# Optimization experiments

Measured on AMD Instinct MI355X. Metric: run time of the kernel, lower is better.

The kernel has to match this reference:

```python
import jax, jax.numpy as jnp
import numpy as np

N_ROIS = 1024
C, H, W = 512, 38, 50           # VGG16 conv5 feature map for a 608x800 image (stride 16)
IMG_H, IMG_W = 608.0, 800.0
POOLING_SIZE = 7                 # cfg.POOLING_SIZE


def setup_inputs() -> dict:
    key = jax.random.key(0)
    k1, k2 = jax.random.split(key, 2)
    bottom = jax.random.normal(k1, (1, C, H, W), dtype=jnp.float32)
    # Build valid ROI boxes (batch_idx, x1, y1, x2, y2) in image coordinates.
    u = jax.random.uniform(k2, (N_ROIS, 4), dtype=jnp.float32)
    x1 = u[:, 0] * (IMG_W - 32.0)
    y1 = u[:, 1] * (IMG_H - 32.0)
    x2 = x1 + 16.0 + u[:, 2] * (IMG_W - 16.0 - x1)
    y2 = y1 + 16.0 + u[:, 3] * (IMG_H - 16.0 - y1)
    rois = jnp.stack([jnp.zeros(N_ROIS, jnp.float32), x1, y1, x2, y2], axis=1)
    return {"bottom": bottom, "rois": rois, "pooling_size": POOLING_SIZE}


def _crop_pool(bottom, rois, pooling_size):
    """Faithful jax version of Network._crop_pool_layer (max_pool=True).
    affine_grid + grid_sample use align_corners=True semantics (old PyTorch
    default, which this theta parameterization assumes) with zeros padding.
    """
    Cc, Hh, Ww = bottom.shape[1], bottom.shape[2], bottom.shape[3]
    pre = pooling_size * 2
    x1 = rois[:, 1] / 16.0
    y1 = rois[:, 2] / 16.0
    x2 = rois[:, 3] / 16.0
    y2 = rois[:, 4] / 16.0
    # theta (separable: grid-x depends only on output col, grid-y only on row)
    t00 = (x2 - x1) / (Ww - 1)
    t02 = (x1 + x2 - Ww + 1) / (Ww - 1)
    t11 = (y2 - y1) / (Hh - 1)
    t12 = (y1 + y2 - Hh + 1) / (Hh - 1)
    base = jnp.linspace(-1.0, 1.0, pre)                 # align_corners=True base grid
    gx = t00[:, None] * base[None, :] + t02[:, None]     # [N, pre] normalized x
    gy = t11[:, None] * base[None, :] + t12[:, None]     # [N, pre] normalized y
    ix = (gx + 1.0) * 0.5 * (Ww - 1)                     # input pixel coords
    iy = (gy + 1.0) * 0.5 * (Hh - 1)
    x0 = jnp.floor(ix)
    y0 = jnp.floor(iy)
    ax = ix - x0
    ay = iy - y0
    x0i = x0.astype(jnp.int32); x1i = x0i + 1
    y0i = y0.astype(jnp.int32); y1i = y0i + 1

    def clip_w(idx, w, size):  # zeros-padding: out-of-bounds corners contribute 0
        valid = (idx >= 0) & (idx <= size - 1)
        return jnp.clip(idx, 0, size - 1), jnp.where(valid, w, 0.0)

    x0c, wx0 = clip_w(x0i, 1.0 - ax, Ww)
    x1c, wx1 = clip_w(x1i, ax, Ww)
    y0c, wy0 = clip_w(y0i, 1.0 - ay, Hh)
    y1c, wy1 = clip_w(y1i, ay, Hh)

    imgf = bottom[0].reshape(Cc, Hh * Ww)               # single image, expanded in torch

    def corner(yc, xc, wy, wx):
        idx = yc[:, :, None] * Ww + xc[:, None, :]      # [N, pre, pre]
        v = jnp.take(imgf, idx, axis=1)                 # [C, N, pre, pre]
        return v * (wy[:, :, None] * wx[:, None, :])[None]

    crops = (corner(y0c, x0c, wy0, wx0) + corner(y0c, x1c, wy0, wx1)
             + corner(y1c, x0c, wy1, wx0) + corner(y1c, x1c, wy1, wx1))
    crops = jnp.transpose(crops, (1, 0, 2, 3))          # [N, C, pre, pre]
    n = rois.shape[0]
    # F.max_pool2d(crops, 2, 2)
    pooled = crops.reshape(n, Cc, pooling_size, 2, pooling_size, 2).max(axis=(3, 5))
    return pooled


def reference(bottom, rois, pooling_size):
    return _crop_pool(bottom, rois, pooling_size)
```

## Files before the change

### kernel.cpp

```cpp
#include <hip/hip_runtime.h>
#include <hip/hip_fp16.h>
#include <float.h>

#define C_    512
#define H_    38
#define W_    50
#define HW_   (H_ * W_)
#define NROIS 1024
#define PS    7
#define PRE   14
#define NCELL 49
#define CQ    128
#define NGP   (PRE * PRE)

typedef float vfloat4 __attribute__((ext_vector_type(4)));
typedef _Float16 h2 __attribute__((ext_vector_type(2)));

__device__ inline h2 bch2(int v)   { return __builtin_bit_cast(h2, v); }
__device__ inline h2 bch2u(unsigned v) { return __builtin_bit_cast(h2, v); }
__device__ inline int bcint(h2 v)  { return __builtin_bit_cast(int, v); }

__global__ __launch_bounds__(256) void transpose_kernel(
    const float* __restrict__ in, _Float16* __restrict__ out) {
    __shared__ float tile[32][33];
    const int pix0 = blockIdx.x * 32;
    const int c0   = blockIdx.y * 32;
    const int tx = threadIdx.x & 31;
    const int ty = threadIdx.x >> 5;

    for (int i = ty; i < 32; i += 8) {
        int c = c0 + i, pix = pix0 + tx;
        tile[i][tx] = (pix < HW_) ? in[c * HW_ + pix] : 0.0f;
    }
    __syncthreads();
    for (int i = ty; i < 32; i += 8) {
        int pix = pix0 + i, c = c0 + tx;
        if (pix < HW_) out[pix * C_ + c] = (_Float16)tile[tx][i];
    }
}

__global__ __launch_bounds__(256, 8) void croppool_kernel(
    const _Float16* __restrict__ src, const float* __restrict__ rois,
    float* __restrict__ out) {

    const int n  = blockIdx.x >> 2;
    const int cq = blockIdx.x & 3;
    const int cbase = cq * CQ;
    const int tid = threadIdx.x;

    __shared__ _Float16 outtile[CQ * NCELL];
    __shared__ int4  offt[NGP];
    __shared__ uint4 wgtt[NGP];

    if (tid < NGP) {
        const int gy = tid / PRE, gx = tid - PRE * gy;
        const float rx1 = rois[n * 5 + 1] * 0.0625f;
        const float ry1 = rois[n * 5 + 2] * 0.0625f;
        const float rx2 = rois[n * 5 + 3] * 0.0625f;
        const float ry2 = rois[n * 5 + 4] * 0.0625f;

        int xi0, xi1, yi0, yi1;
        float wx0, wx1, wy0, wy1;
        {
            const float sz = (float)(W_ - 1);
            const float t0 = (rx2 - rx1) / sz, tc = (rx1 + rx2 - sz) / sz;
            const float base = -1.0f + (float)gx * (2.0f / 13.0f);
            const float coord = (t0 * base + tc + 1.0f) * 0.5f * sz;
            const float f = floorf(coord), a = coord - f;
            const int i0 = (int)f, i1 = i0 + 1;
            wx0 = (i0 >= 0 && i0 <= W_ - 1) ? (1.0f - a) : 0.0f;
            wx1 = (i1 >= 0 && i1 <= W_ - 1) ? a : 0.0f;
            xi0 = min(max(i0, 0), W_ - 1);
            xi1 = min(max(i1, 0), W_ - 1);
        }
        {
            const float sz = (float)(H_ - 1);
            const float t0 = (ry2 - ry1) / sz, tc = (ry1 + ry2 - sz) / sz;
            const float base = -1.0f + (float)gy * (2.0f / 13.0f);
            const float coord = (t0 * base + tc + 1.0f) * 0.5f * sz;
            const float f = floorf(coord), a = coord - f;
            const int i0 = (int)f, i1 = i0 + 1;
            wy0 = (i0 >= 0 && i0 <= H_ - 1) ? (1.0f - a) : 0.0f;
            wy1 = (i1 >= 0 && i1 <= H_ - 1) ? a : 0.0f;
            yi0 = min(max(i0, 0), H_ - 1);
            yi1 = min(max(i1, 0), H_ - 1);
        }
        offt[tid] = make_int4((yi0 * W_ + xi0) * C_, (yi0 * W_ + xi1) * C_,
                              (yi1 * W_ + xi0) * C_, (yi1 * W_ + xi1) * C_);
        const _Float16 w0 = (_Float16)(wy0 * wx0);
        const _Float16 w1 = (_Float16)(wy0 * wx1);
        const _Float16 w2 = (_Float16)(wy1 * wx0);
        const _Float16 w3 = (_Float16)(wy1 * wx1);
        uint4 wv;
        wv.x = __builtin_bit_cast(unsigned, (h2){w0, w0});
        wv.y = __builtin_bit_cast(unsigned, (h2){w1, w1});
        wv.z = __builtin_bit_cast(unsigned, (h2){w2, w2});
        wv.w = __builtin_bit_cast(unsigned, (h2){w3, w3});
        wgtt[tid] = wv;
    }
    __syncthreads();

    const int m    = tid & 15;
    const int q    = (tid >> 4) & 3;
    const int wave = tid >> 6;
    const _Float16* srcc = src + cbase + 8 * m;

    for (int cell = wave; cell < NCELL; cell += 4) {
        const int py = cell / PS, px = cell - PS * py;
        const int gp = (2 * py + (q >> 1)) * PRE + 2 * px + (q & 1);

        const int4  o  = offt[gp];
        const uint4 wv = wgtt[gp];
        const h2 w0 = bch2u(wv.x), w1 = bch2u(wv.y);
        const h2 w2 = bch2u(wv.z), w3 = bch2u(wv.w);

        const uint4 v0 = *(const uint4*)(srcc + o.x);
        const uint4 v1 = *(const uint4*)(srcc + o.y);
        const uint4 v2 = *(const uint4*)(srcc + o.z);
        const uint4 v3 = *(const uint4*)(srcc + o.w);

        h2 a0 = w0 * bch2u(v0.x) + w1 * bch2u(v1.x) + w2 * bch2u(v2.x) + w3 * bch2u(v3.x);
        h2 a1 = w0 * bch2u(v0.y) + w1 * bch2u(v1.y) + w2 * bch2u(v2.y) + w3 * bch2u(v3.y);
        h2 a2 = w0 * bch2u(v0.z) + w1 * bch2u(v1.z) + w2 * bch2u(v2.z) + w3 * bch2u(v3.z);
        h2 a3 = w0 * bch2u(v0.w) + w1 * bch2u(v1.w) + w2 * bch2u(v2.w) + w3 * bch2u(v3.w);

        #pragma unroll
        for (int s = 16; s <= 32; s <<= 1) {
            a0 = __builtin_elementwise_max(a0, bch2(__shfl_xor(bcint(a0), s, 64)));
            a1 = __builtin_elementwise_max(a1, bch2(__shfl_xor(bcint(a1), s, 64)));
            a2 = __builtin_elementwise_max(a2, bch2(__shfl_xor(bcint(a2), s, 64)));
            a3 = __builtin_elementwise_max(a3, bch2(__shfl_xor(bcint(a3), s, 64)));
        }

        const h2 sel = (q == 0) ? a0 : (q == 1) ? a1 : (q == 2) ? a2 : a3;
        const int c0 = 8 * m + 2 * q;
        outtile[c0 * NCELL + cell]       = sel.x;
        outtile[(c0 + 1) * NCELL + cell] = sel.y;
    }
    __syncthreads();

    float* dstb = out + (size_t)n * (C_ * NCELL) + cbase * NCELL;
    const uint4* lsrc = (const uint4*)outtile;
    for (int g = tid; g < CQ * NCELL / 8; g += 256) {
        const uint4 p = lsrc[g];
        vfloat4 lo, hi;
        h2 h;
        h = bch2u(p.x); lo[0] = (float)h.x; lo[1] = (float)h.y;
        h = bch2u(p.y); lo[2] = (float)h.x; lo[3] = (float)h.y;
        h = bch2u(p.z); hi[0] = (float)h.x; hi[1] = (float)h.y;
        h = bch2u(p.w); hi[2] = (float)h.x; hi[3] = (float)h.y;
        __builtin_nontemporal_store(lo, (vfloat4*)(dstb + 8 * g));
        __builtin_nontemporal_store(hi, (vfloat4*)(dstb + 8 * g + 4));
    }
}

__global__ __launch_bounds__(256) void croppool_fallback(
    const float* __restrict__ src, const float* __restrict__ rois,
    float* __restrict__ out) {

    const int n  = blockIdx.x >> 2;
    const int cq = blockIdx.x & 3;
    const int cbase = cq * CQ;
    const int tid = threadIdx.x;

    __shared__ float outtile[CQ * NCELL];
    __shared__ int   xi0[PRE], xi1[PRE], yi0[PRE], yi1[PRE];
    __shared__ float xw0[PRE], xw1[PRE], yw0[PRE], yw1[PRE];

    if (tid < 2 * PRE) {
        const int  j   = tid % PRE;
        const bool isy = tid >= PRE;
        const float r1 = rois[n * 5 + (isy ? 2 : 1)] * 0.0625f;
        const float r2 = rois[n * 5 + (isy ? 4 : 3)] * 0.0625f;
        const float sz = isy ? (float)(H_ - 1) : (float)(W_ - 1);
        const int  szi = isy ? (H_ - 1) : (W_ - 1);
        const float t0 = (r2 - r1) / sz;
        const float tc = (r1 + r2 - sz) / sz;
        const float base = -1.0f + (float)j * (2.0f / 13.0f);
        const float coord = (t0 * base + tc + 1.0f) * 0.5f * sz;
        const float f = floorf(coord);
        const float a = coord - f;
        const int i0 = (int)f;
        const int i1 = i0 + 1;
        const float w0 = (i0 >= 0 && i0 <= szi) ? (1.0f - a) : 0.0f;
        const float w1 = (i1 >= 0 && i1 <= szi) ? a : 0.0f;
        const int i0c = min(max(i0, 0), szi);
        const int i1c = min(max(i1, 0), szi);
        if (isy) { yi0[j] = i0c; yi1[j] = i1c; yw0[j] = w0; yw1[j] = w1; }
        else     { xi0[j] = i0c; xi1[j] = i1c; xw0[j] = w0; xw1[j] = w1; }
    }
    __syncthreads();

    const int wave = tid >> 6;
    const int lane = tid & 63;
    const float* srcc = src + (size_t)(cbase + lane) * HW_;

    for (int cell = wave; cell < NCELL; cell += 4) {
        const int py = cell / PS, px = cell % PS;
        float m0 = -FLT_MAX, m1 = -FLT_MAX;
        for (int ry = 0; ry < 2; ++ry) {
            const int gy = 2 * py + ry;
            for (int rx = 0; rx < 2; ++rx) {
                const int gx = 2 * px + rx;
                const int i00 = yi0[gy] * W_ + xi0[gx], i01 = yi0[gy] * W_ + xi1[gx];
                const int i10 = yi1[gy] * W_ + xi0[gx], i11 = yi1[gy] * W_ + xi1[gx];
                const float v0 = yw0[gy] * (xw0[gx] * srcc[i00] + xw1[gx] * srcc[i01])
                               + yw1[gy] * (xw0[gx] * srcc[i10] + xw1[gx] * srcc[i11]);
                const float v1 = yw0[gy] * (xw0[gx] * srcc[64 * HW_ + i00] + xw1[gx] * srcc[64 * HW_ + i01])
                               + yw1[gy] * (xw0[gx] * srcc[64 * HW_ + i10] + xw1[gx] * srcc[64 * HW_ + i11]);
                m0 = fmaxf(m0, v0);
                m1 = fmaxf(m1, v1);
            }
        }
        outtile[lane * NCELL + cell]        = m0;
        outtile[(lane + 64) * NCELL + cell] = m1;
    }
    __syncthreads();

    const vfloat4* lsrc = (const vfloat4*)outtile;
    vfloat4* dst = (vfloat4*)out + (size_t)n * (C_ * NCELL / 4) + cq * (CQ * NCELL / 4);
    for (int i = tid; i < CQ * NCELL / 4; i += 256) {
        __builtin_nontemporal_store(lsrc[i], &dst[i]);
    }
}

extern "C" void kernel_launch(void* const* d_in, const int* in_sizes, int n_in,
                              void* d_out, int out_size, void* d_ws, size_t ws_size,
                              hipStream_t stream) {
    const float* bottom = (const float*)d_in[0];
    const float* rois   = (const float*)d_in[1];
    float* out = (float*)d_out;

    const size_t trans_bytes = (size_t)HW_ * C_ * sizeof(_Float16);
    if (ws_size >= trans_bytes) {
        _Float16* trans = (_Float16*)d_ws;
        dim3 tgrid((HW_ + 31) / 32, C_ / 32);
        transpose_kernel<<<tgrid, 256, 0, stream>>>(bottom, trans);
        croppool_kernel<<<NROIS * 4, 256, 0, stream>>>(trans, rois, out);
    } else {
        croppool_fallback<<<NROIS * 4, 256, 0, stream>>>(bottom, rois, out);
    }
}
```

Baseline: 46.56 us.

## Process one ROI per 512-thread block with in-thread 2x2 max pooling

The crop-pool kernel now gives each block a whole ROI across all 512 channels with 512 threads, where each lane owns 8 channels and computes all four bilinear samples of a pooling cell itself. This replaces the cross-lane shuffle max reduction and removes the 4x redundant per-block grid/weight setup across channel quarters. The output tile is stored cell-major in a padded LDS buffer and transposed on write-out with scalar fp32 nontemporal stores. The trade-offs are higher register pressure from 16 outstanding 16-byte loads per iteration, scalar rather than vector global stores, and fewer, larger blocks.

```diff
diff --git a/kernel.cpp b/kernel.cpp
--- a/kernel.cpp
+++ b/kernel.cpp
@@ -10,15 +10,14 @@
 #define PS    7
 #define PRE   14
 #define NCELL 49
-#define CQ    128
 #define NGP   (PRE * PRE)
+#define OTP   516
 
 typedef float vfloat4 __attribute__((ext_vector_type(4)));
 typedef _Float16 h2 __attribute__((ext_vector_type(2)));
 
-__device__ inline h2 bch2(int v)   { return __builtin_bit_cast(h2, v); }
-__device__ inline h2 bch2u(unsigned v) { return __builtin_bit_cast(h2, v); }
-__device__ inline int bcint(h2 v)  { return __builtin_bit_cast(int, v); }
+__device__ inline h2 bch2u(unsigned v)   { return __builtin_bit_cast(h2, v); }
+__device__ inline unsigned bcu(h2 v)     { return __builtin_bit_cast(unsigned, v); }
 
 __global__ __launch_bounds__(256) void transpose_kernel(
     const float* __restrict__ in, _Float16* __restrict__ out) {
@@ -39,16 +38,14 @@
     }
 }
 
-__global__ __launch_bounds__(256, 8) void croppool_kernel(
+__global__ __launch_bounds__(512, 4) void croppool_kernel(
     const _Float16* __restrict__ src, const float* __restrict__ rois,
     float* __restrict__ out) {
 
-    const int n  = blockIdx.x >> 2;
-    const int cq = blockIdx.x & 3;
-    const int cbase = cq * CQ;
+    const int n   = blockIdx.x;
     const int tid = threadIdx.x;
 
-    __shared__ _Float16 outtile[CQ * NCELL];
+    __shared__ _Float16 outtile[NCELL * OTP];
     __shared__ int4  offt[NGP];
     __shared__ uint4 wgtt[NGP];
 
@@ -92,65 +89,97 @@
         const _Float16 w2 = (_Float16)(wy1 * wx0);
         const _Float16 w3 = (_Float16)(wy1 * wx1);
         uint4 wv;
-        wv.x = __builtin_bit_cast(unsigned, (h2){w0, w0});
-        wv.y = __builtin_bit_cast(unsigned, (h2){w1, w1});
-        wv.z = __builtin_bit_cast(unsigned, (h2){w2, w2});
-        wv.w = __builtin_bit_cast(unsigned, (h2){w3, w3});
+        wv.x = bcu((h2){w0, w0});
+        wv.y = bcu((h2){w1, w1});
+        wv.z = bcu((h2){w2, w2});
+        wv.w = bcu((h2){w3, w3});
         wgtt[tid] = wv;
     }
     __syncthreads();
 
-    const int m    = tid & 15;
-    const int q    = (tid >> 4) & 3;
+    const int lane = tid & 63;
     const int wave = tid >> 6;
-    const _Float16* srcc = src + cbase + 8 * m;
-
-    for (int cell = wave; cell < NCELL; cell += 4) {
+    const _Float16* srcc = src + 8 * lane;
+
+    for (int cell = wave; cell < NCELL; cell += 8) {
         const int py = cell / PS, px = cell - PS * py;
-        const int gp = (2 * py + (q >> 1)) * PRE + 2 * px + (q & 1);
-
-        const int4  o  = offt[gp];
-        const uint4 wv = wgtt[gp];
-        const h2 w0 = bch2u(wv.x), w1 = bch2u(wv.y);
-        const h2 w2 = bch2u(wv.z), w3 = bch2u(wv.w);
-
-        const uint4 v0 = *(const uint4*)(srcc + o.x);
-        const uint4 v1 = *(const uint4*)(srcc + o.y);
-        const uint4 v2 = *(const uint4*)(srcc + o.z);
-        const uint4 v3 = *(const uint4*)(srcc + o.w);
-
-        h2 a0 = w0 * bch2u(v0.x) + w1 * bch2u(v1.x) + w2 * bch2u(v2.x) + w3 * bch2u(v3.x);
-        h2 a1 = w0 * bch2u(v0.y) + w1 * bch2u(v1.y) + w2 * bch2u(v2.y) + w3 * bch2u(v3.y);
-        h2 a2 = w0 * bch2u(v0.z) + w1 * bch2u(v1.z) + w2 * bch2u(v2.z) + w3 * bch2u(v3.z);
-        h2 a3 = w0 * bch2u(v0.w) + w1 * bch2u(v1.w) + w2 * bch2u(v2.w) + w3 * bch2u(v3.w);
-
-        #pragma unroll
-        for (int s = 16; s <= 32; s <<= 1) {
-            a0 = __builtin_elementwise_max(a0, bch2(__shfl_xor(bcint(a0), s, 64)));
-            a1 = __builtin_elementwise_max(a1, bch2(__shfl_xor(bcint(a1), s, 64)));
-            a2 = __builtin_elementwise_max(a2, bch2(__shfl_xor(bcint(a2), s, 64)));
-            a3 = __builtin_elementwise_max(a3, bch2(__shfl_xor(bcint(a3), s, 64)));
-        }
-
-        const h2 sel = (q == 0) ? a0 : (q == 1) ? a1 : (q == 2) ? a2 : a3;
-        const int c0 = 8 * m + 2 * q;
-        outtile[c0 * NCELL + cell]       = sel.x;
-        outtile[(c0 + 1) * NCELL + cell] = sel.y;
-    }
-    __syncthreads();
-
-    float* dstb = out + (size_t)n * (C_ * NCELL) + cbase * NCELL;
-    const uint4* lsrc = (const uint4*)outtile;
-    for (int g = tid; g < CQ * NCELL / 8; g += 256) {
-        const uint4 p = lsrc[g];
-        vfloat4 lo, hi;
-        h2 h;
-        h = bch2u(p.x); lo[0] = (float)h.x; lo[1] = (float)h.y;
-        h = bch2u(p.y); lo[2] = (float)h.x; lo[3] = (float)h.y;
-        h = bch2u(p.z); hi[0] = (float)h.x; hi[1] = (float)h.y;
-        h = bch2u(p.w); hi[2] = (float)h.x; hi[3] = (float)h.y;
-        __builtin_nontemporal_store(lo, (vfloat4*)(dstb + 8 * g));
-        __builtin_nontemporal_store(hi, (vfloat4*)(dstb + 8 * g + 4));
+        const int gb = 2 * py * PRE + 2 * px;
+        const int gps0 = gb, gps1 = gb + 1, gps2 = gb + PRE, gps3 = gb + PRE + 1;
+
+        uint4 WV0 = wgtt[gps0], WV1 = wgtt[gps1], WV2 = wgtt[gps2], WV3 = wgtt[gps3];
+        const int4 o0 = offt[gps0], o1 = offt[gps1], o2 = offt[gps2], o3 = offt[gps3];
+        const uint4 V00 = *(const uint4*)(srcc + o0.x);
+        const uint4 V01 = *(const uint4*)(srcc + o0.y);
+        const uint4 V02 = *(const uint4*)(srcc + o0.z);
+        const uint4 V03 = *(const uint4*)(srcc + o0.w);
+        const uint4 V10 = *(const uint4*)(srcc + o1.x);
+        const uint4 V11 = *(const uint4*)(srcc + o1.y);
+        const uint4 V12 = *(const uint4*)(srcc + o1.z);
+        const uint4 V13 = *(const uint4*)(srcc + o1.w);
+        const uint4 V20 = *(const uint4*)(srcc + o2.x);
+        const uint4 V21 = *(const uint4*)(srcc + o2.y);
+        const uint4 V22 = *(const uint4*)(srcc + o2.z);
+        const uint4 V23 = *(const uint4*)(srcc + o2.w);
+        const uint4 V30 = *(const uint4*)(srcc + o3.x);
+        const uint4 V31 = *(const uint4*)(srcc + o3.y);
+        const uint4 V32 = *(const uint4*)(srcc + o3.z);
+        const uint4 V33 = *(const uint4*)(srcc + o3.w);
+
+        h2 m0, m1, m2, m3;
+        {
+            const h2 w0 = bch2u(WV0.x), w1 = bch2u(WV0.y), w2 = bch2u(WV0.z), w3 = bch2u(WV0.w);
+            m0 = w0 * bch2u(V00.x) + w1 * bch2u(V01.x) + w2 * bch2u(V02.x) + w3 * bch2u(V03.x);
+            m1 = w0 * bch2u(V00.y) + w1 * bch2u(V01.y) + w2 * bch2u(V02.y) + w3 * bch2u(V03.y);
+            m2 = w0 * bch2u(V00.z) + w1 * bch2u(V01.z) + w2 * bch2u(V02.z) + w3 * bch2u(V03.z);
+            m3 = w0 * bch2u(V00.w) + w1 * bch2u(V01.w) + w2 * bch2u(V02.w) + w3 * bch2u(V03.w);
+        }
+        {
+            const h2 w0 = bch2u(WV1.x), w1 = bch2u(WV1.y), w2 = bch2u(WV1.z), w3 = bch2u(WV1.w);
+            const h2 a0 = w0 * bch2u(V10.x) + w1 * bch2u(V11.x) + w2 * bch2u(V12.x) + w3 * bch2u(V13.x);
+            const h2 a1 = w0 * bch2u(V10.y) + w1 * bch2u(V11.y) + w2 * bch2u(V12.y) + w3 * bch2u(V13.y);
+            const h2 a2 = w0 * bch2u(V10.z) + w1 * bch2u(V11.z) + w2 * bch2u(V12.z) + w3 * bch2u(V13.z);
+            const h2 a3 = w0 * bch2u(V10.w) + w1 * bch2u(V11.w) + w2 * bch2u(V12.w) + w3 * bch2u(V13.w);
+            m0 = __builtin_elementwise_max(m0, a0);
+            m1 = __builtin_elementwise_max(m1, a1);
+            m2 = __builtin_elementwise_max(m2, a2);
+            m3 = __builtin_elementwise_max(m3, a3);
+        }
+        {
+            const h2 w0 = bch2u(WV2.x), w1 = bch2u(WV2.y), w2 = bch2u(WV2.z), w3 = bch2u(WV2.w);
+            const h2 a0 = w0 * bch2u(V20.x) + w1 * bch2u(V21.x) + w2 * bch2u(V22.x) + w3 * bch2u(V23.x);
+            const h2 a1 = w0 * bch2u(V20.y) + w1 * bch2u(V21.y) + w2 * bch2u(V22.y) + w3 * bch2u(V23.y);
+            const h2 a2 = w0 * bch2u(V20.z) + w1 * bch2u(V21.z) + w2 * bch2u(V22.z) + w3 * bch2u(V23.z);
+            const h2 a3 = w0 * bch2u(V20.w) + w1 * bch2u(V21.w) + w2 * bch2u(V22.w) + w3 * bch2u(V23.w);
+            m0 = __builtin_elementwise_max(m0, a0);
+            m1 = __builtin_elementwise_max(m1, a1);
+            m2 = __builtin_elementwise_max(m2, a2);
+            m3 = __builtin_elementwise_max(m3, a3);
+        }
+        {
+            const h2 w0 = bch2u(WV3.x), w1 = bch2u(WV3.y), w2 = bch2u(WV3.z), w3 = bch2u(WV3.w);
+            const h2 a0 = w0 * bch2u(V30.x) + w1 * bch2u(V31.x) + w2 * bch2u(V32.x) + w3 * bch2u(V33.x);
+            const h2 a1 = w0 * bch2u(V30.y) + w1 * bch2u(V31.y) + w2 * bch2u(V32.y) + w3 * bch2u(V33.y);
+            const h2 a2 = w0 * bch2u(V30.z) + w1 * bch2u(V31.z) + w2 * bch2u(V32.z) + w3 * bch2u(V33.z);
+            const h2 a3 = w0 * bch2u(V30.w) + w1 * bch2u(V31.w) + w2 * bch2u(V32.w) + w3 * bch2u(V33.w);
+            m0 = __builtin_elementwise_max(m0, a0);
+            m1 = __builtin_elementwise_max(m1, a1);
+            m2 = __builtin_elementwise_max(m2, a2);
+            m3 = __builtin_elementwise_max(m3, a3);
+        }
+
+        _Float16* dst = &outtile[cell * OTP + 8 * lane];
+        uint2 lo, hi;
+        lo.x = bcu(m0); lo.y = bcu(m1);
+        hi.x = bcu(m2); hi.y = bcu(m3);
+        *(uint2*)dst       = lo;
+        *(uint2*)(dst + 4) = hi;
+    }
+    __syncthreads();
+
+    float* dstb = out + (size_t)n * (C_ * NCELL);
+    for (int f = tid; f < C_ * NCELL; f += 512) {
+        const int c = f / NCELL, cell = f - NCELL * c;
+        __builtin_nontemporal_store((float)outtile[cell * OTP + c], &dstb[f]);
     }
 }
 
@@ -160,10 +189,10 @@
 
     const int n  = blockIdx.x >> 2;
     const int cq = blockIdx.x & 3;
-    const int cbase = cq * CQ;
+    const int cbase = cq * 128;
     const int tid = threadIdx.x;
 
-    __shared__ float outtile[CQ * NCELL];
+    __shared__ float outtile[128 * NCELL];
     __shared__ int   xi0[PRE], xi1[PRE], yi0[PRE], yi1[PRE];
     __shared__ float xw0[PRE], xw1[PRE], yw0[PRE], yw1[PRE];
 
@@ -218,8 +247,8 @@
     __syncthreads();
 
     const vfloat4* lsrc = (const vfloat4*)outtile;
-    vfloat4* dst = (vfloat4*)out + (size_t)n * (C_ * NCELL / 4) + cq * (CQ * NCELL / 4);
-    for (int i = tid; i < CQ * NCELL / 4; i += 256) {
+    vfloat4* dst = (vfloat4*)out + (size_t)n * (C_ * NCELL / 4) + cq * (128 * NCELL / 4);
+    for (int i = tid; i < 128 * NCELL / 4; i += 256) {
         __builtin_nontemporal_store(lsrc[i], &dst[i]);
     }
 }
@@ -236,7 +265,7 @@
         _Float16* trans = (_Float16*)d_ws;
         dim3 tgrid((HW_ + 31) / 32, C_ / 32);
         transpose_kernel<<<tgrid, 256, 0, stream>>>(bottom, trans);
-        croppool_kernel<<<NROIS * 4, 256, 0, stream>>>(trans, rois, out);
+        croppool_kernel<<<NROIS, 512, 0, stream>>>(trans, rois, out);
     } else {
         croppool_fallback<<<NROIS * 4, 256, 0, stream>>>(bottom, rois, out);
     }
```

Result: faster. 43.09 us (-7.4%).
